# Kernel tuning notes

Measured on AMD Instinct MI355X. Metric: run time of the kernel, lower is better.

The kernel has to match this reference:

```python
import jax, jax.numpy as jnp
import numpy as np

B, T, D, H = 4, 4096, 4096, 128  # head_size = embedding_size // num_heads = 4096 // 32

def setup_inputs() -> dict:
    key = jax.random.key(0)
    kx, kq, kk, kv = jax.random.split(key, 4)
    x = jax.random.normal(kx, (B, T, D), dtype=jnp.float32)
    # Dense kernels (no bias), init scale 0.01 as in the module
    Wq = jax.random.normal(kq, (D, H), dtype=jnp.float32) * 0.01
    Wk = jax.random.normal(kk, (D, H), dtype=jnp.float32) * 0.01
    Wv = jax.random.normal(kv, (D, H), dtype=jnp.float32) * 0.01
    return {"x": x, "Wq": Wq, "Wk": Wk, "Wv": Wv}

def reference(x, Wq, Wk, Wv):
    # Single-head projections: (B,T,D) @ (D,H) -> (B,T,H)
    Q = jnp.einsum('btd,dh->bth', x, Wq)
    K = jnp.einsum('btd,dh->bth', x, Wk)
    V = jnp.einsum('btd,dh->bth', x, Wv)
    scale = 1.0 / jnp.sqrt(jnp.asarray(H, dtype=Q.dtype))
    scores = jnp.einsum('bth,bsh->bts', Q, K) * scale  # (B,T,S) full score matrix
    weights = jax.nn.softmax(scores, axis=-1)
    # dropout rate = 0.0 (deterministic/eval) -> identity
    out = jnp.einsum('bts,bsh->bth', weights, V)  # (B,T,H)
    return out
```

## Files before the change

### kernel.cpp

```cpp
#include <hip/hip_runtime.h>


typedef __bf16 bf16_t;
typedef bf16_t bf16x8 __attribute__((ext_vector_type(8)));
typedef float f32x4 __attribute__((ext_vector_type(4)));
typedef float f32x8 __attribute__((ext_vector_type(8)));

#define MFMA16(A, B, C) __builtin_amdgcn_mfma_f32_16x16x32_bf16((A), (B), (C), 0, 0, 0)

__device__ __forceinline__ void async_cp16(const bf16_t* g, bf16_t* lds) {
  __builtin_amdgcn_global_load_lds(
      (__attribute__((address_space(1))) unsigned int*)g,
      (__attribute__((address_space(3))) unsigned int*)lds, 16, 0, 0);
}

__global__ void tr_w(const float* __restrict__ w0, const float* __restrict__ w1,
                     const float* __restrict__ w2, bf16_t* __restrict__ wt) {
  __shared__ float tile[32][33];
  const int z = blockIdx.z;
  const float* src = (z == 0) ? w0 : (z == 1) ? w1 : w2;
  bf16_t* dst = wt + (size_t)z * 128 * 4096;
  const int c0 = blockIdx.x * 32;
  const int r0 = blockIdx.y * 32;
  const int tx = threadIdx.x, ty = threadIdx.y;
#pragma unroll
  for (int j = 0; j < 4; ++j)
    tile[ty + 8 * j][tx] = src[(size_t)(r0 + ty + 8 * j) * 128 + c0 + tx];
  __syncthreads();
#pragma unroll
  for (int j = 0; j < 4; ++j)
    dst[(size_t)(c0 + ty + 8 * j) * 4096 + r0 + tx] = (bf16_t)tile[tx][ty + 8 * j];
}

__global__ void tr_v(const bf16_t* __restrict__ v, bf16_t* __restrict__ vt) {
  __shared__ bf16_t tile[32][33];
  const int b = blockIdx.z;
  const bf16_t* src = v + (size_t)b * 4096 * 128;
  bf16_t* dst = vt + (size_t)b * 128 * 4096;
  const int c0 = blockIdx.x * 32;
  const int r0 = blockIdx.y * 32;
  const int tx = threadIdx.x, ty = threadIdx.y;
#pragma unroll
  for (int j = 0; j < 4; ++j)
    tile[ty + 8 * j][tx] = src[(size_t)(r0 + ty + 8 * j) * 128 + c0 + tx];
  __syncthreads();
#pragma unroll
  for (int j = 0; j < 4; ++j)
    dst[(size_t)(c0 + ty + 8 * j) * 4096 + r0 + tx] = tile[tx][ty + 8 * j];
}

__device__ __forceinline__ void stage_b(const bf16_t* __restrict__ wt_k,
                                        bf16_t* sBbuf, int tid) {
#pragma unroll
  for (int r = 0; r < 3; ++r) {
    int cid = r * 256 + tid;
    int n = cid >> 3, pc = cid & 7;
    int lc = pc ^ (n & 7);
    async_cp16(wt_k + (size_t)n * 4096 + lc * 8, sBbuf + (size_t)cid * 8);
  }
}

__launch_bounds__(256, 4)
__global__ void qkv_proj(const float* __restrict__ x, const bf16_t* __restrict__ wt,
                         bf16_t* __restrict__ q, bf16_t* __restrict__ k,
                         bf16_t* __restrict__ v) {
  __shared__ __align__(16) bf16_t sA[2][64 * 64];
  __shared__ __align__(16) bf16_t sB[2][96 * 64];
  const int tid = threadIdx.x;
  const int w = tid >> 6, lane = tid & 63, lq = lane & 15, quad = lane >> 4;
  const int wr = w >> 1, wc = w & 1;
  const int mblk = (int)blockIdx.x >> 2;
  const int nblk = (int)blockIdx.x & 3;
  const int m0 = mblk * 64;
  const bf16_t* wtb = wt + (size_t)nblk * 96 * 4096;

  int arow[2], apc[2], alc[2];
#pragma unroll
  for (int r = 0; r < 2; ++r) {
    int ca = r * 256 + tid;
    arow[r] = ca >> 3;
    apc[r] = ca & 7;
    alc[r] = apc[r] ^ (arow[r] & 7);
  }
  const float* xb = x + (size_t)m0 * 4096;

  f32x4 acc[2][3];
#pragma unroll
  for (int i = 0; i < 2; ++i)
#pragma unroll
    for (int j = 0; j < 3; ++j) acc[i][j] = (f32x4){0.f, 0.f, 0.f, 0.f};

  float4 fA[4];
#define LOADA(KT)                                                              \
  {                                                                            \
    _Pragma("unroll") for (int r = 0; r < 2; ++r) {                            \
      const float4* p =                                                        \
          (const float4*)(xb + (size_t)arow[r] * 4096 + (KT)*64 + alc[r] * 8); \
      fA[2 * r] = p[0];                                                        \
      fA[2 * r + 1] = p[1];                                                    \
    }                                                                          \
  }

  LOADA(0);
  stage_b(wtb, sB[0], tid);
  __builtin_amdgcn_sched_barrier(0);
#pragma unroll
  for (int r = 0; r < 2; ++r) {
    f32x8 ff = {fA[2 * r].x, fA[2 * r].y, fA[2 * r].z, fA[2 * r].w,
                fA[2 * r + 1].x, fA[2 * r + 1].y, fA[2 * r + 1].z, fA[2 * r + 1].w};
    *(bf16x8*)(sA[0] + arow[r] * 64 + apc[r] * 8) = __builtin_convertvector(ff, bf16x8);
  }
  LOADA(1);
  asm volatile("s_waitcnt vmcnt(4) lgkmcnt(0)" ::: "memory");
  __builtin_amdgcn_s_barrier();

  for (int kt = 0; kt < 64; ++kt) {
    const int buf = kt & 1;
    const int ktB = (kt < 63) ? kt + 1 : 63;
    stage_b(wtb + ktB * 64, sB[buf ^ 1], tid);
    __builtin_amdgcn_sched_barrier(0);
#pragma unroll
    for (int r = 0; r < 2; ++r) {
      f32x8 ff = {fA[2 * r].x, fA[2 * r].y, fA[2 * r].z, fA[2 * r].w,
                  fA[2 * r + 1].x, fA[2 * r + 1].y, fA[2 * r + 1].z, fA[2 * r + 1].w};
      *(bf16x8*)(sA[buf ^ 1] + arow[r] * 64 + apc[r] * 8) =
          __builtin_convertvector(ff, bf16x8);
    }
    const int ktA = (kt < 62) ? kt + 2 : 63;
    LOADA(ktA);
    __builtin_amdgcn_sched_barrier(0);
#pragma unroll
    for (int ks = 0; ks < 2; ++ks) {
      bf16x8 af[2], bfr[3];
      const int cc = ks * 4 + quad;
#pragma unroll
      for (int mt = 0; mt < 2; ++mt) {
        int row = wr * 32 + mt * 16 + lq;
        af[mt] = *(const bf16x8*)(sA[buf] + row * 64 + ((cc ^ (row & 7)) << 3));
      }
#pragma unroll
      for (int nt = 0; nt < 3; ++nt) {
        int n = wc * 48 + nt * 16 + lq;
        bfr[nt] = *(const bf16x8*)(sB[buf] + n * 64 + ((cc ^ (n & 7)) << 3));
      }
#pragma unroll
      for (int mt = 0; mt < 2; ++mt)
#pragma unroll
        for (int nt = 0; nt < 3; ++nt) acc[mt][nt] = MFMA16(af[mt], bfr[nt], acc[mt][nt]);
    }
    asm volatile("s_waitcnt vmcnt(4) lgkmcnt(0)" ::: "memory");
    __builtin_amdgcn_s_barrier();
  }
#undef LOADA

#pragma unroll
  for (int mt = 0; mt < 2; ++mt) {
#pragma unroll
    for (int nt = 0; nt < 3; ++nt) {
      int n = nblk * 96 + wc * 48 + nt * 16 + lq;
      bf16_t* dst;
      int nn;
      if (n < 128) { dst = q; nn = n; }
      else if (n < 256) { dst = k; nn = n - 128; }
      else { dst = v; nn = n - 256; }
#pragma unroll
      for (int r = 0; r < 4; ++r) {
        int m = m0 + wr * 32 + mt * 16 + quad * 4 + r;
        dst[(size_t)m * 128 + nn] = (bf16_t)acc[mt][nt][r];
      }
    }
  }
}

__device__ __forceinline__ void stage_kv(const bf16_t* __restrict__ ksrc,
                                         const bf16_t* __restrict__ vsrc,
                                         bf16_t* sKbuf, bf16_t* sVbuf, int tid) {
#pragma unroll
  for (int r = 0; r < 4; ++r) {
    int cid = r * 256 + tid;
    int row = cid >> 4, pc = cid & 15;
    int lc = pc ^ (row & 15);
    async_cp16(ksrc + row * 128 + lc * 8, sKbuf + (size_t)cid * 8);
  }
#pragma unroll
  for (int r = 0; r < 4; ++r) {
    int cid = r * 256 + tid;
    int h = cid >> 3, pc = cid & 7;
    int lc = pc ^ (h & 7);
    async_cp16(vsrc + (size_t)h * 4096 + lc * 8, sVbuf + (size_t)cid * 8);
  }
}

__launch_bounds__(256, 2)
__global__ void flash(const bf16_t* __restrict__ q, const bf16_t* __restrict__ kk,
                      const bf16_t* __restrict__ vt, float* __restrict__ opart,
                      float* __restrict__ mlm, float* __restrict__ mll) {
  __shared__ __align__(16) bf16_t sK[2][64 * 128];
  __shared__ __align__(16) bf16_t sV[2][128 * 64];
  __shared__ __align__(16) bf16_t sP[64 * 72];
  const int tid = threadIdx.x;
  const int w = tid >> 6, lane = tid & 63, lq = lane & 15, quad = lane >> 4;
  const int b = blockIdx.x & 3;
  const int qt = (blockIdx.x >> 2) & 63;
  const int sp = blockIdx.x >> 8;
  const int qrow0 = qt * 64;

  bf16x8 qf[4];
  {
    const bf16_t* qp = q + ((size_t)b * 4096 + qrow0 + w * 16 + lq) * 128 + quad * 8;
#pragma unroll
    for (int ks = 0; ks < 4; ++ks) qf[ks] = *(const bf16x8*)(qp + ks * 32);
  }

  f32x4 accO[8];
#pragma unroll
  for (int i = 0; i < 8; ++i) accO[i] = (f32x4){0.f, 0.f, 0.f, 0.f};
  float mrow[4] = {-1e30f, -1e30f, -1e30f, -1e30f};
  float lrow[4] = {0.f, 0.f, 0.f, 0.f};

  const bf16_t* kbase = kk + (size_t)b * 4096 * 128;
  const bf16_t* vbase = vt + (size_t)b * 128 * 4096;
  const float SCL = 0.08838834764831845f * 1.4426950408889634f;
  const int it0 = sp * 32;

  stage_kv(kbase + (size_t)it0 * 64 * 128, vbase + it0 * 64, sK[0], sV[0], tid);
  __syncthreads();

  for (int i = 0; i < 32; ++i) {
    const int buf = i & 1;
    if (i < 31)
      stage_kv(kbase + (size_t)(it0 + i + 1) * 64 * 128, vbase + (it0 + i + 1) * 64,
               sK[buf ^ 1], sV[buf ^ 1], tid);

    f32x4 accS[4];
#pragma unroll
    for (int nt = 0; nt < 4; ++nt) accS[nt] = (f32x4){0.f, 0.f, 0.f, 0.f};
    __builtin_amdgcn_s_setprio(1);
#pragma unroll
    for (int ks = 0; ks < 4; ++ks) {
      const int cc = ks * 4 + quad;
#pragma unroll
      for (int nt = 0; nt < 4; ++nt) {
        int row = nt * 16 + lq;
        bf16x8 kf = *(const bf16x8*)(sK[buf] + row * 128 + ((cc ^ (row & 15)) << 3));
        accS[nt] = MFMA16(qf[ks], kf, accS[nt]);
      }
    }
    __builtin_amdgcn_s_setprio(0);

    float mxs[4];
#pragma unroll
    for (int r = 0; r < 4; ++r) {
      float t0 = fmaxf(fmaxf(accS[0][r], accS[1][r]), fmaxf(accS[2][r], accS[3][r]));
#pragma unroll
      for (int msk = 1; msk < 16; msk <<= 1) t0 = fmaxf(t0, __shfl_xor(t0, msk));
      mxs[r] = t0 * SCL;
    }
    bool grow = (mxs[0] > mrow[0]) || (mxs[1] > mrow[1]) ||
                (mxs[2] > mrow[2]) || (mxs[3] > mrow[3]);
    if (__any(grow)) {
      float al[4];
#pragma unroll
      for (int r = 0; r < 4; ++r) {
        float mn = fmaxf(mrow[r], mxs[r]);
        al[r] = exp2f(mrow[r] - mn);
        mrow[r] = mn;
        lrow[r] *= al[r];
      }
#pragma unroll
      for (int ot = 0; ot < 8; ++ot) {
        accO[ot][0] *= al[0]; accO[ot][1] *= al[1];
        accO[ot][2] *= al[2]; accO[ot][3] *= al[3];
      }
    }
    float ps[4] = {0.f, 0.f, 0.f, 0.f};
#pragma unroll
    for (int nt = 0; nt < 4; ++nt)
#pragma unroll
      for (int r = 0; r < 4; ++r) {
        float p = exp2f(fmaf(accS[nt][r], SCL, -mrow[r]));
        accS[nt][r] = p;
        ps[r] += p;
      }
#pragma unroll
    for (int r = 0; r < 4; ++r) {
      float s = ps[r];
#pragma unroll
      for (int msk = 1; msk < 16; msk <<= 1) s += __shfl_xor(s, msk);
      lrow[r] += s;
    }

#pragma unroll
    for (int nt = 0; nt < 4; ++nt) {
      int key = nt * 16 + lq;
#pragma unroll
      for (int r = 0; r < 4; ++r) {
        int prow = w * 16 + quad * 4 + r;
        sP[prow * 72 + key] = (bf16_t)accS[nt][r];
      }
    }

    __builtin_amdgcn_s_setprio(1);
#pragma unroll
    for (int ks2 = 0; ks2 < 2; ++ks2) {
      const int cc = ks2 * 4 + quad;
      bf16x8 pf = *(const bf16x8*)(sP + (w * 16 + lq) * 72 + cc * 8);
#pragma unroll
      for (int ot = 0; ot < 8; ++ot) {
        int h = ot * 16 + lq;
        bf16x8 vf = *(const bf16x8*)(sV[buf] + h * 64 + ((cc ^ (h & 7)) << 3));
        accO[ot] = MFMA16(pf, vf, accO[ot]);
      }
    }
    __builtin_amdgcn_s_setprio(0);
    __syncthreads();
  }

  float* op = opart + ((size_t)(sp * 4 + b) * 4096 + qrow0 + w * 16) * 128;
#pragma unroll
  for (int ot = 0; ot < 8; ++ot)
#pragma unroll
    for (int r = 0; r < 4; ++r)
      op[(size_t)(quad * 4 + r) * 128 + ot * 16 + lq] = accO[ot][r];
  if (lq == 0) {
#pragma unroll
    for (int r = 0; r < 4; ++r) {
      size_t idx = (size_t)(sp * 4 + b) * 4096 + qrow0 + w * 16 + quad * 4 + r;
      mlm[idx] = mrow[r];
      mll[idx] = lrow[r];
    }
  }
}

__global__ void merge(const float* __restrict__ opart, const float* __restrict__ mlm,
                      const float* __restrict__ mll, float* __restrict__ out) {
  const int idx = blockIdx.x * 256 + threadIdx.x;
  const int h = idx & 127;
  const int row = idx >> 7;
  float m0 = mlm[row], m1 = mlm[16384 + row];
  float l0 = mll[row], l1 = mll[16384 + row];
  float M = fmaxf(m0, m1);
  float w0 = exp2f(m0 - M), w1 = exp2f(m1 - M);
  float L = w0 * l0 + w1 * l1;
  float acc = w0 * opart[(size_t)row * 128 + h] +
              w1 * opart[((size_t)16384 + row) * 128 + h];
  out[idx] = acc / L;
}

extern "C" void kernel_launch(void* const* d_in, const int* in_sizes, int n_in,
                              void* d_out, int out_size, void* d_ws, size_t ws_size,
                              hipStream_t stream) {
  (void)in_sizes; (void)n_in; (void)out_size; (void)ws_size;
  const float* x  = (const float*)d_in[0];
  const float* wq = (const float*)d_in[1];
  const float* wk = (const float*)d_in[2];
  const float* wv = (const float*)d_in[3];

  char* ws = (char*)d_ws;
  bf16_t* wt  = (bf16_t*)ws;                         ws += (size_t)384 * 4096 * 2;
  bf16_t* qb  = (bf16_t*)ws;                         ws += (size_t)16384 * 128 * 2;
  bf16_t* kb  = (bf16_t*)ws;                         ws += (size_t)16384 * 128 * 2;
  bf16_t* vb  = (bf16_t*)ws;                         ws += (size_t)16384 * 128 * 2;
  bf16_t* vtb = (bf16_t*)ws;                         ws += (size_t)16384 * 128 * 2;
  float*  opart = (float*)ws;                        ws += (size_t)2 * 16384 * 128 * 4;
  float*  mlm = (float*)ws;                          ws += (size_t)2 * 16384 * 4;
  float*  mll = (float*)ws;
  float*  ob  = (float*)d_out;

  dim3 tb(32, 8, 1);
  tr_w<<<dim3(4, 128, 3), tb, 0, stream>>>(wq, wk, wv, wt);
  qkv_proj<<<dim3(1024), dim3(256), 0, stream>>>(x, wt, qb, kb, vb);
  tr_v<<<dim3(4, 128, 4), tb, 0, stream>>>(vb, vtb);
  flash<<<dim3(512), dim3(256), 0, stream>>>(qb, kb, vtb, opart, mlm, mll);
  merge<<<dim3(8192), dim3(256), 0, stream>>>(opart, mlm, mll, ob);
}
```

Baseline: 568.9 us.

## Use full-width split-K QKV projection tiles and fuse V transpose into reduction

The projection kernel now computes all 384 output columns per block with 128-row tiles and splits K in two, so each fp32 x tile is read once instead of four times. Partial sums go to an fp32 workspace and are reduced by two new kernels: one writes Q/K in bf16 and the other writes V already transposed, replacing the separate V transpose. This trades extra fp32 partial traffic, two extra launches and a single-wave grid with large LDS and register use for much less x traffic.

Result: faster. 506.7 us (-10.9%).

```diff
diff --git a/kernel.cpp b/kernel.cpp
--- a/kernel.cpp
+++ b/kernel.cpp
@@ -2,6 +2,7 @@
 
 
 typedef __bf16 bf16_t;
+typedef bf16_t bf16x4 __attribute__((ext_vector_type(4)));
 typedef bf16_t bf16x8 __attribute__((ext_vector_type(8)));
 typedef float f32x4 __attribute__((ext_vector_type(4)));
 typedef float f32x8 __attribute__((ext_vector_type(8)));
@@ -32,63 +33,45 @@
     dst[(size_t)(c0 + ty + 8 * j) * 4096 + r0 + tx] = (bf16_t)tile[tx][ty + 8 * j];
 }
 
-__global__ void tr_v(const bf16_t* __restrict__ v, bf16_t* __restrict__ vt) {
-  __shared__ bf16_t tile[32][33];
-  const int b = blockIdx.z;
-  const bf16_t* src = v + (size_t)b * 4096 * 128;
-  bf16_t* dst = vt + (size_t)b * 128 * 4096;
-  const int c0 = blockIdx.x * 32;
-  const int r0 = blockIdx.y * 32;
-  const int tx = threadIdx.x, ty = threadIdx.y;
-#pragma unroll
-  for (int j = 0; j < 4; ++j)
-    tile[ty + 8 * j][tx] = src[(size_t)(r0 + ty + 8 * j) * 128 + c0 + tx];
-  __syncthreads();
-#pragma unroll
-  for (int j = 0; j < 4; ++j)
-    dst[(size_t)(c0 + ty + 8 * j) * 4096 + r0 + tx] = tile[tx][ty + 8 * j];
-}
-
-__device__ __forceinline__ void stage_b(const bf16_t* __restrict__ wt_k,
-                                        bf16_t* sBbuf, int tid) {
-#pragma unroll
-  for (int r = 0; r < 3; ++r) {
-    int cid = r * 256 + tid;
+__device__ __forceinline__ void stage_b384(const bf16_t* __restrict__ wt_k,
+                                           bf16_t* sBbuf, int tid) {
+#pragma unroll
+  for (int r = 0; r < 6; ++r) {
+    int cid = r * 512 + tid;
     int n = cid >> 3, pc = cid & 7;
     int lc = pc ^ (n & 7);
     async_cp16(wt_k + (size_t)n * 4096 + lc * 8, sBbuf + (size_t)cid * 8);
   }
 }
 
-__launch_bounds__(256, 4)
-__global__ void qkv_proj(const float* __restrict__ x, const bf16_t* __restrict__ wt,
-                         bf16_t* __restrict__ q, bf16_t* __restrict__ k,
-                         bf16_t* __restrict__ v) {
-  __shared__ __align__(16) bf16_t sA[2][64 * 64];
-  __shared__ __align__(16) bf16_t sB[2][96 * 64];
+__launch_bounds__(512, 1)
+__global__ void qkv_ks(const float* __restrict__ x, const bf16_t* __restrict__ wt,
+                       float* __restrict__ opart) {
+  __shared__ __align__(16) bf16_t sA[2][128 * 64];
+  __shared__ __align__(16) bf16_t sB[2][384 * 64];
   const int tid = threadIdx.x;
   const int w = tid >> 6, lane = tid & 63, lq = lane & 15, quad = lane >> 4;
-  const int wr = w >> 1, wc = w & 1;
-  const int mblk = (int)blockIdx.x >> 2;
-  const int nblk = (int)blockIdx.x & 3;
-  const int m0 = mblk * 64;
-  const bf16_t* wtb = wt + (size_t)nblk * 96 * 4096;
+  const int wr = w >> 2, wc = w & 3;
+  const int mblk = (int)blockIdx.x >> 1;
+  const int sp = (int)blockIdx.x & 1;
+  const int m0 = mblk * 128;
+  const int kt0 = sp * 32;
 
   int arow[2], apc[2], alc[2];
 #pragma unroll
   for (int r = 0; r < 2; ++r) {
-    int ca = r * 256 + tid;
+    int ca = r * 512 + tid;
     arow[r] = ca >> 3;
     apc[r] = ca & 7;
     alc[r] = apc[r] ^ (arow[r] & 7);
   }
   const float* xb = x + (size_t)m0 * 4096;
 
-  f32x4 acc[2][3];
-#pragma unroll
-  for (int i = 0; i < 2; ++i)
-#pragma unroll
-    for (int j = 0; j < 3; ++j) acc[i][j] = (f32x4){0.f, 0.f, 0.f, 0.f};
+  f32x4 acc[4][6];
+#pragma unroll
+  for (int i = 0; i < 4; ++i)
+#pragma unroll
+    for (int j = 0; j < 6; ++j) acc[i][j] = (f32x4){0.f, 0.f, 0.f, 0.f};
 
   float4 fA[4];
 #define LOADA(KT)                                                              \
@@ -101,8 +84,8 @@
     }                                                                          \
   }
 
-  LOADA(0);
-  stage_b(wtb, sB[0], tid);
+  LOADA(kt0);
+  stage_b384(wt + kt0 * 64, sB[0], tid);
   __builtin_amdgcn_sched_barrier(0);
 #pragma unroll
   for (int r = 0; r < 2; ++r) {
@@ -110,14 +93,15 @@
                 fA[2 * r + 1].x, fA[2 * r + 1].y, fA[2 * r + 1].z, fA[2 * r + 1].w};
     *(bf16x8*)(sA[0] + arow[r] * 64 + apc[r] * 8) = __builtin_convertvector(ff, bf16x8);
   }
-  LOADA(1);
+  LOADA(kt0 + 1);
   asm volatile("s_waitcnt vmcnt(4) lgkmcnt(0)" ::: "memory");
   __builtin_amdgcn_s_barrier();
 
-  for (int kt = 0; kt < 64; ++kt) {
-    const int buf = kt & 1;
-    const int ktB = (kt < 63) ? kt + 1 : 63;
-    stage_b(wtb + ktB * 64, sB[buf ^ 1], tid);
+  for (int k2 = 0; k2 < 32; ++k2) {
+    const int kt = kt0 + k2;
+    const int buf = k2 & 1;
+    const int ktB = (k2 < 31) ? kt + 1 : kt;
+    stage_b384(wt + ktB * 64, sB[buf ^ 1], tid);
     __builtin_amdgcn_sched_barrier(0);
 #pragma unroll
     for (int r = 0; r < 2; ++r) {
@@ -126,50 +110,83 @@
       *(bf16x8*)(sA[buf ^ 1] + arow[r] * 64 + apc[r] * 8) =
           __builtin_convertvector(ff, bf16x8);
     }
-    const int ktA = (kt < 62) ? kt + 2 : 63;
+    const int ktA = (k2 < 30) ? kt + 2 : kt0 + 31;
     LOADA(ktA);
     __builtin_amdgcn_sched_barrier(0);
 #pragma unroll
     for (int ks = 0; ks < 2; ++ks) {
-      bf16x8 af[2], bfr[3];
+      bf16x8 af[4], bfr[6];
       const int cc = ks * 4 + quad;
 #pragma unroll
-      for (int mt = 0; mt < 2; ++mt) {
-        int row = wr * 32 + mt * 16 + lq;
+      for (int mt = 0; mt < 4; ++mt) {
+        int row = wr * 64 + mt * 16 + lq;
         af[mt] = *(const bf16x8*)(sA[buf] + row * 64 + ((cc ^ (row & 7)) << 3));
       }
 #pragma unroll
-      for (int nt = 0; nt < 3; ++nt) {
-        int n = wc * 48 + nt * 16 + lq;
+      for (int nt = 0; nt < 6; ++nt) {
+        int n = wc * 96 + nt * 16 + lq;
         bfr[nt] = *(const bf16x8*)(sB[buf] + n * 64 + ((cc ^ (n & 7)) << 3));
       }
 #pragma unroll
-      for (int mt = 0; mt < 2; ++mt)
-#pragma unroll
-        for (int nt = 0; nt < 3; ++nt) acc[mt][nt] = MFMA16(af[mt], bfr[nt], acc[mt][nt]);
+      for (int mt = 0; mt < 4; ++mt)
+#pragma unroll
+        for (int nt = 0; nt < 6; ++nt) acc[mt][nt] = MFMA16(af[mt], bfr[nt], acc[mt][nt]);
     }
     asm volatile("s_waitcnt vmcnt(4) lgkmcnt(0)" ::: "memory");
     __builtin_amdgcn_s_barrier();
   }
 #undef LOADA
 
-#pragma unroll
-  for (int mt = 0; mt < 2; ++mt) {
-#pragma unroll
-    for (int nt = 0; nt < 3; ++nt) {
-      int n = nblk * 96 + wc * 48 + nt * 16 + lq;
-      bf16_t* dst;
-      int nn;
-      if (n < 128) { dst = q; nn = n; }
-      else if (n < 256) { dst = k; nn = n - 128; }
-      else { dst = v; nn = n - 256; }
+  float* op = opart + (size_t)sp * 16384 * 384;
+#pragma unroll
+  for (int mt = 0; mt < 4; ++mt) {
+#pragma unroll
+    for (int nt = 0; nt < 6; ++nt) {
+      int n = wc * 96 + nt * 16 + lq;
 #pragma unroll
       for (int r = 0; r < 4; ++r) {
-        int m = m0 + wr * 32 + mt * 16 + quad * 4 + r;
-        dst[(size_t)m * 128 + nn] = (bf16_t)acc[mt][nt][r];
-      }
-    }
-  }
+        int m = m0 + wr * 64 + mt * 16 + quad * 4 + r;
+        op[(size_t)m * 384 + n] = acc[mt][nt][r];
+      }
+    }
+  }
+}
+
+__global__ void qkred(const float* __restrict__ opart, bf16_t* __restrict__ q,
+                      bf16_t* __restrict__ k) {
+  const int tid = threadIdx.x;
+  const int t = blockIdx.x * 4 + (tid >> 6);
+  const int n4 = (tid & 63) * 4;
+  const float* p0 = opart + (size_t)t * 384 + n4;
+  const float* p1 = p0 + (size_t)16384 * 384;
+  float4 a = *(const float4*)p0, b = *(const float4*)p1;
+  bf16x4 o;
+  o[0] = (bf16_t)(a.x + b.x);
+  o[1] = (bf16_t)(a.y + b.y);
+  o[2] = (bf16_t)(a.z + b.z);
+  o[3] = (bf16_t)(a.w + b.w);
+  if (n4 < 128)
+    *(bf16x4*)(q + (size_t)t * 128 + n4) = o;
+  else
+    *(bf16x4*)(k + (size_t)t * 128 + (n4 - 128)) = o;
+}
+
+__global__ void vred(const float* __restrict__ opart, bf16_t* __restrict__ vt) {
+  __shared__ bf16_t tile[32][33];
+  const int c0 = blockIdx.x * 32;
+  const int t0 = blockIdx.y * 32;
+  const int tx = threadIdx.x, ty = threadIdx.y;
+  const float* p0 = opart + 256;
+  const float* p1 = p0 + (size_t)16384 * 384;
+#pragma unroll
+  for (int j = 0; j < 4; ++j) {
+    size_t idx = (size_t)(t0 + ty + 8 * j) * 384 + c0 + tx;
+    tile[ty + 8 * j][tx] = (bf16_t)(p0[idx] + p1[idx]);
+  }
+  __syncthreads();
+#pragma unroll
+  for (int j = 0; j < 4; ++j)
+    vt[(size_t)(c0 + ty + 8 * j) * 16384 + t0 + tx] = tile[tx][ty + 8 * j];
 }
 
 __device__ __forceinline__ void stage_kv(const bf16_t* __restrict__ ksrc,
@@ -187,7 +204,7 @@
     int cid = r * 256 + tid;
     int h = cid >> 3, pc = cid & 7;
     int lc = pc ^ (h & 7);
-    async_cp16(vsrc + (size_t)h * 4096 + lc * 8, sVbuf + (size_t)cid * 8);
+    async_cp16(vsrc + (size_t)h * 16384 + lc * 8, sVbuf + (size_t)cid * 8);
   }
 }
 
@@ -219,7 +236,7 @@
   float lrow[4] = {0.f, 0.f, 0.f, 0.f};
 
   const bf16_t* kbase = kk + (size_t)b * 4096 * 128;
-  const bf16_t* vbase = vt + (size_t)b * 128 * 4096;
+  const bf16_t* vbase = vt + (size_t)b * 4096;
   const float SCL = 0.08838834764831845f * 1.4426950408889634f;
   const int it0 = sp * 32;
 
@@ -360,8 +377,8 @@
   bf16_t* wt  = (bf16_t*)ws;                         ws += (size_t)384 * 4096 * 2;
   bf16_t* qb  = (bf16_t*)ws;                         ws += (size_t)16384 * 128 * 2;
   bf16_t* kb  = (bf16_t*)ws;                         ws += (size_t)16384 * 128 * 2;
-  bf16_t* vb  = (bf16_t*)ws;                         ws += (size_t)16384 * 128 * 2;
   bf16_t* vtb = (bf16_t*)ws;                         ws += (size_t)16384 * 128 * 2;
+  float*  oqkv = (float*)ws;                         ws += (size_t)2 * 16384 * 384 * 4;
   float*  opart = (float*)ws;                        ws += (size_t)2 * 16384 * 128 * 4;
   float*  mlm = (float*)ws;                          ws += (size_t)2 * 16384 * 4;
   float*  mll = (float*)ws;
@@ -369,8 +386,9 @@
 
   dim3 tb(32, 8, 1);
   tr_w<<<dim3(4, 128, 3), tb, 0, stream>>>(wq, wk, wv, wt);
-  qkv_proj<<<dim3(1024), dim3(256), 0, stream>>>(x, wt, qb, kb, vb);
-  tr_v<<<dim3(4, 128, 4), tb, 0, stream>>>(vb, vtb);
+  qkv_ks<<<dim3(256), dim3(512), 0, stream>>>(x, wt, oqkv);
+  qkred<<<dim3(4096), dim3(256), 0, stream>>>(oqkv, qb, kb);
+  vred<<<dim3(4, 512), tb, 0, stream>>>(oqkv, vtb);
   flash<<<dim3(512), dim3(256), 0, stream>>>(qb, kb, vtb, opart, mlm, mll);
   merge<<<dim3(8192), dim3(256), 0, stream>>>(opart, mlm, mll, ob);
 }
```
